# Kernel tuning notes

Measured on AMD Instinct MI355X. Metric: run time of the kernel, lower is better.

The kernel has to match this reference:

```python
import jax, jax.numpy as jnp
import numpy as np

N_INPUT = 128
N_HIDDEN = 128

def setup_inputs() -> dict:
    key = jax.random.key(0)
    k1, k2, k3, k4, k5 = jax.random.split(key, 5)
    B, T = 64, 4096
    fan1 = N_INPUT + N_HIDDEN
    s1 = 1.0 / np.sqrt(fan1)
    s2 = 1.0 / np.sqrt(N_HIDDEN)
    return {
        "input": jax.random.normal(k1, (B, T, N_INPUT), dtype=jnp.float32),
        "W1": jax.random.uniform(k2, (N_HIDDEN, fan1), jnp.float32, -s1, s1),
        "b1": jax.random.uniform(k3, (N_HIDDEN,), jnp.float32, -s1, s1),
        "W2": jax.random.uniform(k4, (N_HIDDEN, N_HIDDEN), jnp.float32, -s2, s2),
        "b2": jax.random.uniform(k5, (N_HIDDEN,), jnp.float32, -s2, s2),
    }

def reference(input, W1, b1, W2, b2):
    # input: [B, T, n_input]; carried state h: [B, n_hidden]
    B, T, _ = input.shape
    # split linear1 weight: cat order is (h, x)
    W1h = W1[:, :N_HIDDEN]   # [H, H]
    W1x = W1[:, N_HIDDEN:]   # [H, n_input]
    # precompute input projection for all timesteps: [B, T, H]
    x_proj = jnp.einsum('bti,hi->bth', input, W1x) + b1

    def step(h, xp_t):
        h_new = jax.nn.relu(h @ W1h.T + xp_t)          # [B, H]
        out = jax.nn.relu(h_new @ W2.T + b2)            # [B, H]
        return h_new, out

    h0 = jnp.zeros((B, N_HIDDEN), dtype=input.dtype)
    _, outs = jax.lax.scan(step, h0, jnp.swapaxes(x_proj, 0, 1))  # outs: [T, B, H]
    return jnp.swapaxes(outs, 0, 1)  # [B, T, H]
```

## Files before the change

kernel.cpp:

```cpp
#include <hip/hip_runtime.h>
#include <stdint.h>

#define T_LEN 4096
#define NHID  128

typedef float    f32x4 __attribute__((ext_vector_type(4)));
typedef _Float16 f16x4 __attribute__((ext_vector_type(4)));
typedef _Float16 f16x8 __attribute__((ext_vector_type(8)));
typedef __fp16   h16x2 __attribute__((ext_vector_type(2)));
typedef uint32_t u32x2 __attribute__((ext_vector_type(2)));
typedef uint32_t u32x4 __attribute__((ext_vector_type(4)));

struct P2 { h16x2 p0, p1; };
struct P4 { h16x2 p0, p1, p2, p3; };
struct U22 { u32x2 a, b; };

static __device__ __forceinline__ f16x4 cvt_f16x4(f32x4 v) {
    P2 p;
    p.p0 = __builtin_amdgcn_cvt_pkrtz(v.x, v.y);
    p.p1 = __builtin_amdgcn_cvt_pkrtz(v.z, v.w);
    return __builtin_bit_cast(f16x4, p);
}
static __device__ __forceinline__ f16x8 cvt_f16x8(f32x4 a, f32x4 b) {
    P4 p;
    p.p0 = __builtin_amdgcn_cvt_pkrtz(a.x, a.y);
    p.p1 = __builtin_amdgcn_cvt_pkrtz(a.z, a.w);
    p.p2 = __builtin_amdgcn_cvt_pkrtz(b.x, b.y);
    p.p3 = __builtin_amdgcn_cvt_pkrtz(b.z, b.w);
    return __builtin_bit_cast(f16x8, p);
}
static __device__ __forceinline__ f32x4 relu4(f32x4 v) {
    v.x = fmaxf(v.x, 0.f); v.y = fmaxf(v.y, 0.f);
    v.z = fmaxf(v.z, 0.f); v.w = fmaxf(v.w, 0.f);
    return v;
}
static __device__ __forceinline__ u32x2 relu_pk(f32x4 v) {
    P2 p;
    p.p0 = __builtin_amdgcn_cvt_pkrtz(v.x, v.y);
    p.p1 = __builtin_amdgcn_cvt_pkrtz(v.z, v.w);
    f16x4 h = __builtin_bit_cast(f16x4, p);
    const f16x4 z = {};
    h = __builtin_elementwise_max(h, z);
    return __builtin_bit_cast(u32x2, h);
}
static __device__ __forceinline__ f32x4 unpk4(u32x2 q) {
    f16x4 h = __builtin_bit_cast(f16x4, q);
    f32x4 r = { (float)h.x, (float)h.y, (float)h.z, (float)h.w };
    return r;
}
#define MFMA32(a, b, c) __builtin_amdgcn_mfma_f32_16x16x32_f16((a), (b), (c), 0, 0, 0)
#define MFMA16(a, b, c) __builtin_amdgcn_mfma_f32_16x16x16f16((a), (b), (c), 0, 0, 0)

#define LDS_BARRIER()  asm volatile("s_waitcnt lgkmcnt(0)\n\ts_barrier" ::: "memory")
#define BARRIER_ONLY() asm volatile("s_barrier" ::: "memory")


__global__ __launch_bounds__(64, 2)
void xproj_kernel(const float* __restrict__ input, const float* __restrict__ W1,
                  const float* __restrict__ b1, uint32_t* __restrict__ xp) {
    const int bid = blockIdx.x;
    const int g   = bid >> 8;
    const int tc  = bid & 255;
    const int l   = threadIdx.x;
    const int c   = l & 15, u = l >> 4;

    f16x8 wa[8][4];
#pragma unroll
    for (int m = 0; m < 8; ++m) {
        const float* wr = W1 + (16 * m + c) * 256 + 128 + 8 * u;
#pragma unroll
        for (int j = 0; j < 4; ++j)
            wa[m][j] = cvt_f16x8(*(const f32x4*)(wr + 32 * j),
                                 *(const f32x4*)(wr + 32 * j + 4));
    }
    f32x4 bi[8];
#pragma unroll
    for (int m = 0; m < 8; ++m) bi[m] = *(const f32x4*)(b1 + 16 * m + 4 * u);

    const int t0 = tc * 16;
    const float* ip0 = input + (size_t)(16 * g + c) * T_LEN * NHID + 8 * u;
    uint32_t* xp0 = xp + ((size_t)g * T_LEN) * 1024 + 4 * l;
#pragma unroll 1
    for (int tt = 0; tt < 16; ++tt) {
        const int t = t0 + tt;
        const float* ip = ip0 + (size_t)t * NHID;
        f16x8 xb[4];
#pragma unroll
        for (int j = 0; j < 4; ++j)
            xb[j] = cvt_f16x8(*(const f32x4*)(ip + 32 * j),
                              *(const f32x4*)(ip + 32 * j + 4));
        u32x2 pk[8];
#pragma unroll
        for (int m = 0; m < 8; ++m) {
            f32x4 a = bi[m];
#pragma unroll
            for (int j = 0; j < 4; ++j) a = MFMA32(wa[m][j], xb[j], a);
            pk[m] = __builtin_bit_cast(u32x2, cvt_f16x4(a));
        }
        uint32_t* xpt = xp0 + (size_t)t * 1024;
#pragma unroll
        for (int q = 0; q < 4; ++q) {
            U22 qq = { pk[q], pk[q + 4] };
            *(u32x4*)(xpt + q * 256) = __builtin_bit_cast(u32x4, qq);
        }
    }
}

__global__ __launch_bounds__(320, 1)
void rec_kernel(const uint32_t* __restrict__ xp, const float* __restrict__ W1,
                uint32_t* __restrict__ hg) {
    const int g  = blockIdx.x;
    const int wv = threadIdx.x >> 6;
    const int l  = threadIdx.x & 63;
    const int c  = l & 15, u = l >> 4;

    __shared__ uint32_t hbuf[4][1024];

    for (int i = threadIdx.x; i < 1024; i += 320) hbuf[0][i] = 0;
    __syncthreads();

    if (wv < 4) {
        __builtin_amdgcn_s_setprio(1);
        const int w = wv;
        f16x8 waH[2][4];
#pragma unroll
        for (int e = 0; e < 2; ++e) {
            const float* wr = W1 + (16 * (w + 4 * e) + c) * 256;
#pragma unroll
            for (int kt = 0; kt < 4; ++kt)
                waH[e][kt] = cvt_f16x8(*(const f32x4*)(wr + 16 * kt + 4 * u),
                                       *(const f32x4*)(wr + 64 + 16 * kt + 4 * u));
        }

        const uint32_t* xpl = xp + ((size_t)g * T_LEN) * 1024 + w * 256 + 4 * l;

        u32x4 xr[8];
#pragma unroll
        for (int p = 0; p < 8; ++p)
            xr[p] = *(const u32x4*)(xpl + (size_t)p * 1024);

        f16x8 own;
        {
            const u32x4 z = {0, 0, 0, 0};
            own = __builtin_bit_cast(f16x8, z);
        }
        f32x4 xf0, xf1;
        {
            U22 xq = __builtin_bit_cast(U22, xr[0]);
            xf0 = unpk4(xq.a);
            xf1 = unpk4(xq.b);
        }
        const f32x4 zf = { 0.f, 0.f, 0.f, 0.f };
        const int k1 = (w + 1) & 3, k2 = (w + 2) & 3, k3 = (w + 3) & 3;

#pragma unroll 1
        for (int t8 = 0; t8 < T_LEN; t8 += 8) {
#pragma unroll
            for (int p = 0; p < 8; ++p) {
                const int t = t8 + p;
                const uint32_t* rb = &hbuf[p & 3][0];
                u32x4 r1 = *(const u32x4*)&rb[k1 * 256 + 4 * l];
                u32x4 r2 = *(const u32x4*)&rb[k2 * 256 + 4 * l];
                u32x4 r3 = *(const u32x4*)&rb[k3 * 256 + 4 * l];
                f32x4 a0a = MFMA32(waH[0][w], own, xf0);
                f32x4 a1a = MFMA32(waH[1][w], own, xf1);
                {
                    U22 xq = __builtin_bit_cast(U22, xr[(p + 1) & 7]);
                    xf0 = unpk4(xq.a);
                    xf1 = unpk4(xq.b);
                }
                f16x8 b1 = __builtin_bit_cast(f16x8, r1);
                f32x4 a0b = MFMA32(waH[0][k1], b1, zf);
                f32x4 a1b = MFMA32(waH[1][k1], b1, zf);
                f16x8 b2 = __builtin_bit_cast(f16x8, r2);
                a0a = MFMA32(waH[0][k2], b2, a0a);
                a1a = MFMA32(waH[1][k2], b2, a1a);
                f16x8 b3 = __builtin_bit_cast(f16x8, r3);
                a0b = MFMA32(waH[0][k3], b3, a0b);
                a1b = MFMA32(waH[1][k3], b3, a1b);
                u32x2 p0 = relu_pk(a0a + a0b);
                u32x2 p1 = relu_pk(a1a + a1b);
                U22 oq = { p0, p1 };
                own = __builtin_bit_cast(f16x8, oq);
                *(u32x4*)&hbuf[(p + 1) & 3][w * 256 + 4 * l] =
                    __builtin_bit_cast(u32x4, oq);
                int tn = t + 8; if (tn > T_LEN - 1) tn = T_LEN - 1;
                xr[p] = *(const u32x4*)(xpl + (size_t)tn * 1024);
                LDS_BARRIER();
            }
        }
    } else {
        uint32_t* hgp = hg + ((size_t)g * T_LEN) * 1024 + 4 * l;
        u32x4 v[2][8];
#pragma unroll 1
        for (int t8 = 0; t8 < T_LEN; t8 += 8) {
#pragma unroll
            for (int p = 0; p < 8; ++p) {
                const int t = t8 + p;
                if (p & 1) {
                    const int r = (p >> 1) & 1;
                    const uint32_t* rbA = &hbuf[p & 3][0];
                    const uint32_t* rbB = &hbuf[(p - 1) & 3][0];
#pragma unroll
                    for (int q = 0; q < 4; ++q)
                        v[r][q] = *(const u32x4*)&rbA[q * 256 + 4 * l];
#pragma unroll
                    for (int q = 0; q < 4; ++q)
                        v[r][4 + q] = *(const u32x4*)&rbB[q * 256 + 4 * l];
                    uint32_t* hpA = hgp + (size_t)(t - 1) * 1024;
#pragma unroll
                    for (int q = 0; q < 4; ++q)
                        *(u32x4*)(hpA + q * 256) = v[r][q];
                    if (t > 1) {
                        uint32_t* hpB = hgp + (size_t)(t - 2) * 1024;
#pragma unroll
                        for (int q = 0; q < 4; ++q)
                            *(u32x4*)(hpB + q * 256) = v[r][4 + q];
                    }
                }
                BARRIER_ONLY();
            }
        }
        {
            const uint32_t* rb = &hbuf[0][0];
            u32x4 vf[4];
#pragma unroll
            for (int q = 0; q < 4; ++q)
                vf[q] = *(const u32x4*)&rb[q * 256 + 4 * l];
            uint32_t* hp = hgp + (size_t)(T_LEN - 1) * 1024;
#pragma unroll
            for (int q = 0; q < 4; ++q)
                *(u32x4*)(hp + q * 256) = vf[q];
        }
    }
}

__global__ __launch_bounds__(64, 2)
void out_kernel(const uint32_t* __restrict__ hg, const float* __restrict__ W2,
                const float* __restrict__ b2, float* __restrict__ out) {
    const int bid = blockIdx.x;
    const int g   = bid >> 9;
    const int tc  = bid & 511;
    const int l   = threadIdx.x;
    const int c   = l & 15, u = l >> 4;

    f16x4 wa[8][8];
#pragma unroll
    for (int m = 0; m < 8; ++m) {
        const float* wr = W2 + (16 * m + c) * 128 + 4 * u;
#pragma unroll
        for (int s = 0; s < 8; ++s)
            wa[m][s] = cvt_f16x4(*(const f32x4*)(wr + 16 * s));
    }
    f32x4 bi[8];
#pragma unroll
    for (int m = 0; m < 8; ++m) bi[m] = *(const f32x4*)(b2 + 16 * m + 4 * u);

    const int t0 = tc * 8;
    const uint32_t* hg0 = hg + ((size_t)g * T_LEN) * 1024 + 4 * l;
    float* op0 = out + (size_t)(16 * g + c) * T_LEN * NHID + 4 * u;
#pragma unroll 1
    for (int tt = 0; tt < 8; ++tt) {
        const int t = t0 + tt;
        const uint32_t* hp = hg0 + (size_t)t * 1024;
        f16x4 hb[8];
#pragma unroll
        for (int s = 0; s < 8; ++s)
            hb[s] = __builtin_bit_cast(f16x4,
                        *(const u32x2*)(hp + (s & 3) * 256 + (s >> 2) * 2));
        f32x4 acc[8];
#pragma unroll
        for (int m = 0; m < 8; ++m) {
            f32x4 a = bi[m];
#pragma unroll
            for (int s = 0; s < 8; ++s) a = MFMA16(wa[m][s], hb[s], a);
            acc[m] = relu4(a);
        }
        float* op = op0 + (size_t)t * NHID;
#pragma unroll
        for (int m = 0; m < 8; ++m) *(f32x4*)(op + 16 * m) = acc[m];
    }
}

extern "C" void kernel_launch(void* const* d_in, const int* in_sizes, int n_in,
                              void* d_out, int out_size, void* d_ws, size_t ws_size,
                              hipStream_t stream) {
    const float* input = (const float*)d_in[0];
    const float* W1    = (const float*)d_in[1];
    const float* b1    = (const float*)d_in[2];
    const float* W2    = (const float*)d_in[3];
    const float* b2    = (const float*)d_in[4];
    float*    out = (float*)d_out;
    uint32_t* xpb = (uint32_t*)d_out;
    uint32_t* hgb = (uint32_t*)d_ws;

    xproj_kernel<<<1024, 64, 0, stream>>>(input, W1, b1, xpb);
    rec_kernel  <<<4,   320, 0, stream>>>(xpb, W1, hgb);
    out_kernel  <<<2048, 64, 0, stream>>>(hgb, W2, b2, out);
}
```

Before: 1.072 ms.

## Drop store wave in recurrence, write h from compute waves; use K=32 MFMA in output

Removes the fifth writer wave from the recurrent kernel. The four compute waves now keep the last eight hidden states in registers and write them to global memory four steps late. The own-block MFMA for the next step is moved to the end of each iteration so it overlaps with the barrier. Separately, the output kernel switches from 16x16x16 to 16x16x32 f16 MFMA with 128-bit loads, which halves the MFMA count. The risk is that the global stores in the latency-critical loop lengthen each serial step, and that the extra registers raise pressure.

```diff
diff --git a/kernel.cpp b/kernel.cpp
--- a/kernel.cpp
+++ b/kernel.cpp
@@ -49,10 +49,8 @@
     return r;
 }
 #define MFMA32(a, b, c) __builtin_amdgcn_mfma_f32_16x16x32_f16((a), (b), (c), 0, 0, 0)
-#define MFMA16(a, b, c) __builtin_amdgcn_mfma_f32_16x16x16f16((a), (b), (c), 0, 0, 0)
 
 #define LDS_BARRIER()  asm volatile("s_waitcnt lgkmcnt(0)\n\ts_barrier" ::: "memory")
-#define BARRIER_ONLY() asm volatile("s_barrier" ::: "memory")
 
 
 __global__ __launch_bounds__(64, 2)
@@ -106,132 +104,105 @@
     }
 }
 
-__global__ __launch_bounds__(320, 1)
+__global__ __launch_bounds__(256, 1)
 void rec_kernel(const uint32_t* __restrict__ xp, const float* __restrict__ W1,
                 uint32_t* __restrict__ hg) {
-    const int g  = blockIdx.x;
-    const int wv = threadIdx.x >> 6;
-    const int l  = threadIdx.x & 63;
-    const int c  = l & 15, u = l >> 4;
+    const int g = blockIdx.x;
+    const int w = threadIdx.x >> 6;
+    const int l = threadIdx.x & 63;
+    const int c = l & 15, u = l >> 4;
 
     __shared__ uint32_t hbuf[4][1024];
 
-    for (int i = threadIdx.x; i < 1024; i += 320) hbuf[0][i] = 0;
+    for (int i = threadIdx.x; i < 1024; i += 256) hbuf[0][i] = 0;
     __syncthreads();
 
-    if (wv < 4) {
-        __builtin_amdgcn_s_setprio(1);
-        const int w = wv;
-        f16x8 waH[2][4];
-#pragma unroll
-        for (int e = 0; e < 2; ++e) {
-            const float* wr = W1 + (16 * (w + 4 * e) + c) * 256;
-#pragma unroll
-            for (int kt = 0; kt < 4; ++kt)
-                waH[e][kt] = cvt_f16x8(*(const f32x4*)(wr + 16 * kt + 4 * u),
-                                       *(const f32x4*)(wr + 64 + 16 * kt + 4 * u));
-        }
-
-        const uint32_t* xpl = xp + ((size_t)g * T_LEN) * 1024 + w * 256 + 4 * l;
-
-        u32x4 xr[8];
-#pragma unroll
-        for (int p = 0; p < 8; ++p)
-            xr[p] = *(const u32x4*)(xpl + (size_t)p * 1024);
-
-        f16x8 own;
-        {
-            const u32x4 z = {0, 0, 0, 0};
-            own = __builtin_bit_cast(f16x8, z);
-        }
-        f32x4 xf0, xf1;
-        {
-            U22 xq = __builtin_bit_cast(U22, xr[0]);
-            xf0 = unpk4(xq.a);
-            xf1 = unpk4(xq.b);
-        }
-        const f32x4 zf = { 0.f, 0.f, 0.f, 0.f };
-        const int k1 = (w + 1) & 3, k2 = (w + 2) & 3, k3 = (w + 3) & 3;
+    f16x8 waH[2][4];
+#pragma unroll
+    for (int e = 0; e < 2; ++e) {
+        const float* wr = W1 + (16 * (w + 4 * e) + c) * 256;
+#pragma unroll
+        for (int kt = 0; kt < 4; ++kt)
+            waH[e][kt] = cvt_f16x8(*(const f32x4*)(wr + 16 * kt + 4 * u),
+                                   *(const f32x4*)(wr + 64 + 16 * kt + 4 * u));
+    }
+
+    const uint32_t* xpl = xp + ((size_t)g * T_LEN) * 1024 + w * 256 + 4 * l;
+    uint32_t*       hgp = hg + ((size_t)g * T_LEN) * 1024 + w * 256 + 4 * l;
+
+    u32x4 xr[8];
+#pragma unroll
+    for (int p = 0; p < 8; ++p)
+        xr[p] = *(const u32x4*)(xpl + (size_t)p * 1024);
+
+    f16x8 own;
+    {
+        const u32x4 z = {0, 0, 0, 0};
+        own = __builtin_bit_cast(f16x8, z);
+    }
+    f32x4 xf0, xf1, a0a, a1a;
+    {
+        U22 xq = __builtin_bit_cast(U22, xr[0]);
+        xf0 = unpk4(xq.a);
+        xf1 = unpk4(xq.b);
+        a0a = MFMA32(waH[0][w], own, xf0);
+        a1a = MFMA32(waH[1][w], own, xf1);
+        U22 xn = __builtin_bit_cast(U22, xr[1]);
+        xf0 = unpk4(xn.a);
+        xf1 = unpk4(xn.b);
+    }
+    u32x2 pkv[8][2];
+    const f32x4 zf = { 0.f, 0.f, 0.f, 0.f };
+    const int k1 = (w + 1) & 3, k2 = (w + 2) & 3, k3 = (w + 3) & 3;
 
 #pragma unroll 1
-        for (int t8 = 0; t8 < T_LEN; t8 += 8) {
-#pragma unroll
-            for (int p = 0; p < 8; ++p) {
-                const int t = t8 + p;
-                const uint32_t* rb = &hbuf[p & 3][0];
-                u32x4 r1 = *(const u32x4*)&rb[k1 * 256 + 4 * l];
-                u32x4 r2 = *(const u32x4*)&rb[k2 * 256 + 4 * l];
-                u32x4 r3 = *(const u32x4*)&rb[k3 * 256 + 4 * l];
-                f32x4 a0a = MFMA32(waH[0][w], own, xf0);
-                f32x4 a1a = MFMA32(waH[1][w], own, xf1);
-                {
-                    U22 xq = __builtin_bit_cast(U22, xr[(p + 1) & 7]);
-                    xf0 = unpk4(xq.a);
-                    xf1 = unpk4(xq.b);
-                }
-                f16x8 b1 = __builtin_bit_cast(f16x8, r1);
-                f32x4 a0b = MFMA32(waH[0][k1], b1, zf);
-                f32x4 a1b = MFMA32(waH[1][k1], b1, zf);
-                f16x8 b2 = __builtin_bit_cast(f16x8, r2);
-                a0a = MFMA32(waH[0][k2], b2, a0a);
-                a1a = MFMA32(waH[1][k2], b2, a1a);
-                f16x8 b3 = __builtin_bit_cast(f16x8, r3);
-                a0b = MFMA32(waH[0][k3], b3, a0b);
-                a1b = MFMA32(waH[1][k3], b3, a1b);
-                u32x2 p0 = relu_pk(a0a + a0b);
-                u32x2 p1 = relu_pk(a1a + a1b);
-                U22 oq = { p0, p1 };
-                own = __builtin_bit_cast(f16x8, oq);
-                *(u32x4*)&hbuf[(p + 1) & 3][w * 256 + 4 * l] =
-                    __builtin_bit_cast(u32x4, oq);
-                int tn = t + 8; if (tn > T_LEN - 1) tn = T_LEN - 1;
-                xr[p] = *(const u32x4*)(xpl + (size_t)tn * 1024);
-                LDS_BARRIER();
+    for (int t8 = 0; t8 < T_LEN; t8 += 8) {
+#pragma unroll
+        for (int p = 0; p < 8; ++p) {
+            const int t = t8 + p;
+            const uint32_t* rb = &hbuf[p & 3][0];
+            u32x4 r1 = *(const u32x4*)&rb[k1 * 256 + 4 * l];
+            u32x4 r2 = *(const u32x4*)&rb[k2 * 256 + 4 * l];
+            u32x4 r3 = *(const u32x4*)&rb[k3 * 256 + 4 * l];
+            if (t >= 4) {
+                U22 sq = { pkv[(p + 4) & 7][0], pkv[(p + 4) & 7][1] };
+                *(u32x4*)(hgp + (size_t)(t - 4) * 1024) =
+                    __builtin_bit_cast(u32x4, sq);
             }
-        }
-    } else {
-        uint32_t* hgp = hg + ((size_t)g * T_LEN) * 1024 + 4 * l;
-        u32x4 v[2][8];
-#pragma unroll 1
-        for (int t8 = 0; t8 < T_LEN; t8 += 8) {
-#pragma unroll
-            for (int p = 0; p < 8; ++p) {
-                const int t = t8 + p;
-                if (p & 1) {
-                    const int r = (p >> 1) & 1;
-                    const uint32_t* rbA = &hbuf[p & 3][0];
-                    const uint32_t* rbB = &hbuf[(p - 1) & 3][0];
-#pragma unroll
-                    for (int q = 0; q < 4; ++q)
-                        v[r][q] = *(const u32x4*)&rbA[q * 256 + 4 * l];
-#pragma unroll
-                    for (int q = 0; q < 4; ++q)
-                        v[r][4 + q] = *(const u32x4*)&rbB[q * 256 + 4 * l];
-                    uint32_t* hpA = hgp + (size_t)(t - 1) * 1024;
-#pragma unroll
-                    for (int q = 0; q < 4; ++q)
-                        *(u32x4*)(hpA + q * 256) = v[r][q];
-                    if (t > 1) {
-                        uint32_t* hpB = hgp + (size_t)(t - 2) * 1024;
-#pragma unroll
-                        for (int q = 0; q < 4; ++q)
-                            *(u32x4*)(hpB + q * 256) = v[r][4 + q];
-                    }
-                }
-                BARRIER_ONLY();
+            int tn = t + 8; if (tn > T_LEN - 1) tn = T_LEN - 1;
+            xr[p] = *(const u32x4*)(xpl + (size_t)tn * 1024);
+            f16x8 b1 = __builtin_bit_cast(f16x8, r1);
+            f32x4 a0b = MFMA32(waH[0][k1], b1, zf);
+            f32x4 a1b = MFMA32(waH[1][k1], b1, zf);
+            f16x8 b2 = __builtin_bit_cast(f16x8, r2);
+            a0a = MFMA32(waH[0][k2], b2, a0a);
+            a1a = MFMA32(waH[1][k2], b2, a1a);
+            f16x8 b3 = __builtin_bit_cast(f16x8, r3);
+            a0b = MFMA32(waH[0][k3], b3, a0b);
+            a1b = MFMA32(waH[1][k3], b3, a1b);
+            u32x2 p0 = relu_pk(a0a + a0b);
+            u32x2 p1 = relu_pk(a1a + a1b);
+            pkv[p & 7][0] = p0;
+            pkv[p & 7][1] = p1;
+            U22 oq = { p0, p1 };
+            own = __builtin_bit_cast(f16x8, oq);
+            *(u32x4*)&hbuf[(p + 1) & 3][w * 256 + 4 * l] =
+                __builtin_bit_cast(u32x4, oq);
+            a0a = MFMA32(waH[0][w], own, xf0);
+            a1a = MFMA32(waH[1][w], own, xf1);
+            {
+                U22 xq = __builtin_bit_cast(U22, xr[(p + 2) & 7]);
+                xf0 = unpk4(xq.a);
+                xf1 = unpk4(xq.b);
             }
-        }
-        {
-            const uint32_t* rb = &hbuf[0][0];
-            u32x4 vf[4];
-#pragma unroll
-            for (int q = 0; q < 4; ++q)
-                vf[q] = *(const u32x4*)&rb[q * 256 + 4 * l];
-            uint32_t* hp = hgp + (size_t)(T_LEN - 1) * 1024;
-#pragma unroll
-            for (int q = 0; q < 4; ++q)
-                *(u32x4*)(hp + q * 256) = vf[q];
-        }
+            LDS_BARRIER();
+        }
+    }
+#pragma unroll
+    for (int d = 0; d < 4; ++d) {
+        U22 sq = { pkv[(T_LEN - 4 + d) & 7][0], pkv[(T_LEN - 4 + d) & 7][1] };
+        *(u32x4*)(hgp + (size_t)(T_LEN - 4 + d) * 1024) =
+            __builtin_bit_cast(u32x4, sq);
     }
 }
 
@@ -244,13 +215,14 @@
     const int l   = threadIdx.x;
     const int c   = l & 15, u = l >> 4;
 
-    f16x4 wa[8][8];
+    f16x8 wa[8][4];
 #pragma unroll
     for (int m = 0; m < 8; ++m) {
-        const float* wr = W2 + (16 * m + c) * 128 + 4 * u;
-#pragma unroll
-        for (int s = 0; s < 8; ++s)
-            wa[m][s] = cvt_f16x4(*(const f32x4*)(wr + 16 * s));
+        const float* wr = W2 + (16 * m + c) * 128;
+#pragma unroll
+        for (int q = 0; q < 4; ++q)
+            wa[m][q] = cvt_f16x8(*(const f32x4*)(wr + 16 * q + 4 * u),
+                                 *(const f32x4*)(wr + 64 + 16 * q + 4 * u));
     }
     f32x4 bi[8];
 #pragma unroll
@@ -263,17 +235,16 @@
     for (int tt = 0; tt < 8; ++tt) {
         const int t = t0 + tt;
         const uint32_t* hp = hg0 + (size_t)t * 1024;
-        f16x4 hb[8];
-#pragma unroll
-        for (int s = 0; s < 8; ++s)
-            hb[s] = __builtin_bit_cast(f16x4,
-                        *(const u32x2*)(hp + (s & 3) * 256 + (s >> 2) * 2));
+        f16x8 hb[4];
+#pragma unroll
+        for (int q = 0; q < 4; ++q)
+            hb[q] = __builtin_bit_cast(f16x8, *(const u32x4*)(hp + q * 256));
         f32x4 acc[8];
 #pragma unroll
         for (int m = 0; m < 8; ++m) {
             f32x4 a = bi[m];
 #pragma unroll
-            for (int s = 0; s < 8; ++s) a = MFMA16(wa[m][s], hb[s], a);
+            for (int q = 0; q < 4; ++q) a = MFMA32(wa[m][q], hb[q], a);
             acc[m] = relu4(a);
         }
         float* op = op0 + (size_t)t * NHID;
@@ -295,6 +266,6 @@
     uint32_t* hgb = (uint32_t*)d_ws;
 
     xproj_kernel<<<1024, 64, 0, stream>>>(input, W1, b1, xpb);
-    rec_kernel  <<<4,   320, 0, stream>>>(xpb, W1, hgb);
+    rec_kernel  <<<4,   256, 0, stream>>>(xpb, W1, hgb);
     out_kernel  <<<2048, 64, 0, stream>>>(hgb, W2, b2, out);
 }
```

Result: slower. 1.339 ms (+24.8%).
